# Performance work log

Hardware: AMD Instinct MI355X
Metric: run time of the kernel (lower is better)

Reference implementation:

```python
import jax, jax.numpy as jnp
import numpy as np

N, L, S, E, D = 8, 2048, 2048, 1024, 64

def setup_inputs() -> dict:
    key = jax.random.key(0)
    ks = jax.random.split(key, 6)
    q = jax.random.normal(ks[0], (N, L, E), dtype=jnp.float32)
    k = jax.random.normal(ks[1], (N, S, E), dtype=jnp.float32)
    v = jax.random.normal(ks[2], (N, S, E), dtype=jnp.float32)
    # Linear weights stored as [E, D] so projection is x @ W
    Wq = jax.random.normal(ks[3], (E, D), dtype=jnp.float32) / np.sqrt(E)
    Wk = jax.random.normal(ks[4], (E, D), dtype=jnp.float32) / np.sqrt(E)
    Wv = jax.random.normal(ks[5], (E, D), dtype=jnp.float32) / np.sqrt(E)
    # causal bool mask: True above diagonal => masked to -inf
    attn_mask = jnp.triu(jnp.ones((L, S), dtype=bool), k=1)
    return {"q": q, "k": k, "v": v, "Wq": Wq, "Wk": Wk, "Wv": Wv, "attn_mask": attn_mask}


def reference(q, k, v, Wq, Wk, Wv, attn_mask):
    qh = q @ Wq                      # [N, L, D]
    kh = k @ Wk                      # [N, S, D]
    vh = v @ Wv                      # [N, S, D]
    # NOTE: source divides by d**(-1/2), i.e. multiplies by sqrt(D) (faithful bug)
    scale = jnp.asarray(D, dtype=qh.dtype) ** 0.5
    scores = jnp.einsum("nld,nsd->nls", qh, kh) * scale   # [N, L, S]
    scores = jnp.where(attn_mask[None, :, :], -jnp.inf, scores)
    weights = jax.nn.softmax(scores, axis=-1)
    out = jnp.einsum("nls,nsd->nld", weights, vh)          # [N, L, D]
    return out
```

## Files before the change

kernel.cpp:

```cpp
#include <hip/hip_runtime.h>
#include <math.h>

#define NB 8
#define LQ 2048
#define LOG2E 1.44269504088896f

typedef __attribute__((ext_vector_type(4))) float f32x4;
typedef __attribute__((ext_vector_type(8))) short s16x8;

__device__ __forceinline__ unsigned f2bf_u(float f) {
  unsigned u = __builtin_bit_cast(unsigned, f);
  u += 0x7FFFu + ((u >> 16) & 1u);
  return u >> 16;
}
__device__ __forceinline__ float bf2f(unsigned h) {
  unsigned u = h << 16;
  return __builtin_bit_cast(float, u);
}

#define MFMA16 __builtin_amdgcn_mfma_f32_16x16x32_bf16

__global__ __launch_bounds__(256) void wsplit_kernel(
    const float* __restrict__ Wq, const float* __restrict__ Wk,
    const float* __restrict__ Wv, short* __restrict__ wt) {
  int bk = blockIdx.x;
  int z = blockIdx.y;
  const float* W = (z == 0) ? Wq : (z == 1) ? Wk : Wv;
  __shared__ float tile[64][65];
  int t = threadIdx.x;
#pragma unroll
  for (int it = 0; it < 16; ++it) {
    int kk = it * 4 + (t >> 6);
    int d = t & 63;
    tile[kk][d] = W[(size_t)(bk * 64 + kk) * 64 + d];
  }
  __syncthreads();
#pragma unroll
  for (int it = 0; it < 16; ++it) {
    int d = it * 4 + (t >> 6);
    int kk = t & 63;
    float f = tile[kk][d];
    unsigned h = f2bf_u(f);
    unsigned l = f2bf_u(f - bf2f(h));
    wt[((size_t)(z * 2 + 0) * 64 + d) * 1024 + bk * 64 + kk] = (short)h;
    wt[((size_t)(z * 2 + 1) * 64 + d) * 1024 + bk * 64 + kk] = (short)l;
  }
}

__global__ __launch_bounds__(256, 3) void proj_kernel(
    const float* __restrict__ xq, const float* __restrict__ xk,
    const float* __restrict__ xv, const short* __restrict__ wt,
    short* __restrict__ qhi, short* __restrict__ qlo,
    short* __restrict__ khi, short* __restrict__ klo,
    short* __restrict__ vhT) {
  int z = blockIdx.y;
  const float* x = (z == 0) ? xq : (z == 1) ? xk : xv;
  const short* wthi = wt + (size_t)(z * 2 + 0) * 64 * 1024;
  const short* wtlo = wt + (size_t)(z * 2 + 1) * 64 * 1024;
  int row0 = blockIdx.x * 64;
  int t = threadIdx.x;
  int wv = t >> 6, lane = t & 63;
  int c = lane & 15, quad = lane >> 4;

  __shared__ float xa[2][64 * 64];
  __shared__ short vtile[64][72];

  const float* xg = x + (size_t)row0 * 1024;

#define STAGE(buf, kb)                                                        \
  {                                                                           \
    _Pragma("unroll") for (int j = 0; j < 4; ++j) {                           \
      int row = wv * 16 + j * 4 + quad;                                       \
      const float* src = xg + (size_t)row * 1024 + (kb) * 64 +                \
                         ((c ^ (row & 7)) << 2);                              \
      float* dst = &xa[buf][(wv * 4 + j) * 256];       \
      __builtin_amdgcn_global_load_lds(                                       \
          (const __attribute__((address_space(1))) unsigned*)src,             \
          (__attribute__((address_space(3))) unsigned*)dst, 16, 0, 0);        \
    }                                                                         \
  }

  f32x4 acc[4] = {};
  STAGE(0, 0);
  __syncthreads();
  int cur = 0;
  int rowl = wv * 16 + c;
  for (int kb = 0; kb < 16; ++kb) {
    if (kb < 15) STAGE(cur ^ 1, kb + 1);
    s16x8 bh[4][2], bl[4][2];
    int ko = kb * 64 + quad * 8;
#pragma unroll
    for (int cs = 0; cs < 4; ++cs) {
      const short* bp = wthi + (size_t)(cs * 16 + c) * 1024 + ko;
      const short* lp = wtlo + (size_t)(cs * 16 + c) * 1024 + ko;
      bh[cs][0] = *(const s16x8*)(bp);
      bh[cs][1] = *(const s16x8*)(bp + 32);
      bl[cs][0] = *(const s16x8*)(lp);
      bl[cs][1] = *(const s16x8*)(lp + 32);
    }
    const float* arow = &xa[cur][rowl * 64];
#pragma unroll
    for (int kc = 0; kc < 2; ++kc) {
      int ch0 = ((kc * 8 + quad * 2 + 0) ^ (c & 7)) << 2;
      int ch1 = ((kc * 8 + quad * 2 + 1) ^ (c & 7)) << 2;
      f32x4 a0 = *(const f32x4*)(arow + ch0);
      f32x4 a1 = *(const f32x4*)(arow + ch1);
      s16x8 ah, al;
#pragma unroll
      for (int j = 0; j < 4; ++j) {
        unsigned h;
        h = f2bf_u(a0[j]); ah[j] = (short)h;     al[j] = (short)f2bf_u(a0[j] - bf2f(h));
        h = f2bf_u(a1[j]); ah[4 + j] = (short)h; al[4 + j] = (short)f2bf_u(a1[j] - bf2f(h));
      }
#pragma unroll
      for (int cs = 0; cs < 4; ++cs) {
        acc[cs] = MFMA16(ah, bh[cs][kc], acc[cs], 0, 0, 0);
        acc[cs] = MFMA16(ah, bl[cs][kc], acc[cs], 0, 0, 0);
        acc[cs] = MFMA16(al, bh[cs][kc], acc[cs], 0, 0, 0);
      }
    }
    __syncthreads();
    cur ^= 1;
  }
#undef STAGE
  if (z < 2) {
    short* hi = (z == 0) ? qhi : khi;
    short* lo = (z == 0) ? qlo : klo;
#pragma unroll
    for (int cs = 0; cs < 4; ++cs)
#pragma unroll
      for (int r = 0; r < 4; ++r) {
        int row = row0 + wv * 16 + quad * 4 + r;
        int col = cs * 16 + c;
        float val = acc[cs][r];
        unsigned h = f2bf_u(val);
        unsigned l = f2bf_u(val - bf2f(h));
        hi[(size_t)row * 64 + col] = (short)h;
        lo[(size_t)row * 64 + col] = (short)l;
      }
  } else {
#pragma unroll
    for (int cs = 0; cs < 4; ++cs)
#pragma unroll
      for (int r = 0; r < 4; ++r)
        vtile[cs * 16 + c][wv * 16 + quad * 4 + r] = (short)f2bf_u(acc[cs][r]);
    __syncthreads();
    int n = row0 >> 11;
    int sbase = row0 & 2047;
    int d = t >> 2, sc = (t & 3) * 16;
#pragma unroll
    for (int j = 0; j < 2; ++j) {
      s16x8 vv = *(const s16x8*)&vtile[d][sc + j * 8];
      *(s16x8*)&vhT[((size_t)n * 64 + d) * LQ + sbase + sc + j * 8] = vv;
    }
  }
}

__global__ __launch_bounds__(256, 3) void attn_kernel(
    const short* __restrict__ qhi, const short* __restrict__ qlo,
    const short* __restrict__ khi, const short* __restrict__ klo,
    const short* __restrict__ vhT, float* __restrict__ outp) {
  int bid = blockIdx.x;
  int n = bid & 7;
  int qt = 127 - (bid >> 3);
  int t = threadIdx.x;
  int wv = t >> 6, lane = t & 63;
  int c = lane & 15, quad = lane >> 4;
  int qr0 = qt * 16;
  __shared__ short pS[4][16][72];
  __shared__ float mS[4][16], lS[4][16];
  __shared__ float oS[4][16][64];
  s16x8 qfh[2], qfl[2];
  size_t qbase = ((size_t)n * LQ + qr0 + c) * 64;
#pragma unroll
  for (int kc = 0; kc < 2; ++kc) {
    qfh[kc] = *(const s16x8*)&qhi[qbase + kc * 32 + quad * 8];
    qfl[kc] = *(const s16x8*)&qlo[qbase + kc * 32 + quad * 8];
  }
  f32x4 o[4] = {};
  float m_r[4], l_r[4];
#pragma unroll
  for (int r = 0; r < 4; ++r) { m_r[r] = -INFINITY; l_r[r] = 0.0f; }
  int ktmax = qt >> 2;
  for (int kt = wv; kt <= ktmax; kt += 4) {
    int s0 = kt * 64;
    size_t kbase = ((size_t)n * LQ + s0) * 64;
    f32x4 sa[4] = {};
#pragma unroll
    for (int ct = 0; ct < 4; ++ct) {
      size_t rb = kbase + (size_t)(ct * 16 + c) * 64;
#pragma unroll
      for (int kc = 0; kc < 2; ++kc) {
        s16x8 bh = *(const s16x8*)&khi[rb + kc * 32 + quad * 8];
        s16x8 bl = *(const s16x8*)&klo[rb + kc * 32 + quad * 8];
        sa[ct] = MFMA16(qfh[kc], bh, sa[ct], 0, 0, 0);
        sa[ct] = MFMA16(qfh[kc], bl, sa[ct], 0, 0, 0);
        sa[ct] = MFMA16(qfl[kc], bh, sa[ct], 0, 0, 0);
      }
    }
    s16x8 vb[4][2];
#pragma unroll
    for (int dt = 0; dt < 4; ++dt)
#pragma unroll
      for (int kc2 = 0; kc2 < 2; ++kc2)
        vb[dt][kc2] = *(const s16x8*)&vhT[((size_t)n * 64 + dt * 16 + c) * LQ +
                                          s0 + kc2 * 32 + quad * 8];
    float sv[4][4];
    bool diag = (kt == ktmax);
#pragma unroll
    for (int ct = 0; ct < 4; ++ct)
#pragma unroll
      for (int r = 0; r < 4; ++r) {
        float xsc = sa[ct][r] * 8.0f;
        if (diag) {
          int sg = s0 + ct * 16 + c;
          int qg = qr0 + quad * 4 + r;
          if (sg > qg) xsc = -INFINITY;
        }
        sv[ct][r] = xsc;
      }
    float alpha[4];
#pragma unroll
    for (int r = 0; r < 4; ++r) {
      float mx = fmaxf(fmaxf(sv[0][r], sv[1][r]), fmaxf(sv[2][r], sv[3][r]));
#pragma unroll
      for (int off = 1; off < 16; off <<= 1) mx = fmaxf(mx, __shfl_xor(mx, off, 64));
      float mnew = fmaxf(m_r[r], mx);
      alpha[r] = exp2f((m_r[r] - mnew) * LOG2E);
      m_r[r] = mnew;
      float rs = 0.0f;
#pragma unroll
      for (int ct = 0; ct < 4; ++ct) {
        float p = exp2f((sv[ct][r] - mnew) * LOG2E);
        sv[ct][r] = p;
        rs += p;
      }
#pragma unroll
      for (int off = 1; off < 16; off <<= 1) rs += __shfl_xor(rs, off, 64);
      l_r[r] = l_r[r] * alpha[r] + rs;
    }
#pragma unroll
    for (int dt = 0; dt < 4; ++dt)
#pragma unroll
      for (int r = 0; r < 4; ++r) o[dt][r] *= alpha[r];
#pragma unroll
    for (int ct = 0; ct < 4; ++ct)
#pragma unroll
      for (int r = 0; r < 4; ++r)
        pS[wv][quad * 4 + r][ct * 16 + c] = (short)f2bf_u(sv[ct][r]);
    s16x8 pa[2];
#pragma unroll
    for (int kc2 = 0; kc2 < 2; ++kc2)
      pa[kc2] = *(const s16x8*)&pS[wv][c][kc2 * 32 + quad * 8];
#pragma unroll
    for (int dt = 0; dt < 4; ++dt)
#pragma unroll
      for (int kc2 = 0; kc2 < 2; ++kc2)
        o[dt] = MFMA16(pa[kc2], vb[dt][kc2], o[dt], 0, 0, 0);
  }
#pragma unroll
  for (int dt = 0; dt < 4; ++dt)
#pragma unroll
    for (int r = 0; r < 4; ++r)
      oS[wv][quad * 4 + r][dt * 16 + c] = o[dt][r];
  if (c == 0) {
#pragma unroll
    for (int r = 0; r < 4; ++r) {
      mS[wv][quad * 4 + r] = m_r[r];
      lS[wv][quad * 4 + r] = l_r[r];
    }
  }
  __syncthreads();
  {
    int r = t >> 4;
    int c4 = (t & 15) * 4;
    float m0 = mS[0][r], m1 = mS[1][r], m2 = mS[2][r], m3 = mS[3][r];
    float mstar = fmaxf(fmaxf(m0, m1), fmaxf(m2, m3));
    float s0 = exp2f((m0 - mstar) * LOG2E);
    float s1 = exp2f((m1 - mstar) * LOG2E);
    float s2 = exp2f((m2 - mstar) * LOG2E);
    float s3 = exp2f((m3 - mstar) * LOG2E);
    float lstar = s0 * lS[0][r] + s1 * lS[1][r] + s2 * lS[2][r] + s3 * lS[3][r];
    float inv = 1.0f / lstar;
    f32x4 oa;
#pragma unroll
    for (int j = 0; j < 4; ++j)
      oa[j] = (s0 * oS[0][r][c4 + j] + s1 * oS[1][r][c4 + j] +
               s2 * oS[2][r][c4 + j] + s3 * oS[3][r][c4 + j]) * inv;
    *(f32x4*)&outp[((size_t)n * LQ + qr0 + r) * 64 + c4] = oa;
  }
}

extern "C" void kernel_launch(void* const* d_in, const int* in_sizes, int n_in,
                              void* d_out, int out_size, void* d_ws, size_t ws_size,
                              hipStream_t stream) {
  const float* q = (const float*)d_in[0];
  const float* k = (const float*)d_in[1];
  const float* v = (const float*)d_in[2];
  const float* Wq = (const float*)d_in[3];
  const float* Wk = (const float*)d_in[4];
  const float* Wv = (const float*)d_in[5];
  float* out = (float*)d_out;

  char* ws = (char*)d_ws;
  short* wt  = (short*)ws;
  short* qhi = (short*)(ws + 786432);
  short* qlo = qhi + (size_t)16384 * 64;
  short* khi = qlo + (size_t)16384 * 64;
  short* klo = khi + (size_t)16384 * 64;
  short* vhT = klo + (size_t)16384 * 64;

  wsplit_kernel<<<dim3(16, 3), 256, 0, stream>>>(Wq, Wk, Wv, wt);
  proj_kernel<<<dim3(256, 3), 256, 0, stream>>>(q, k, v, wt, qhi, qlo, khi, klo, vhT);
  attn_kernel<<<dim3(1024), 256, 0, stream>>>(qhi, qlo, khi, klo, vhT, out);
}
```

Baseline: 310.3 us.

## Pre-swizzle split weights and stage them through shared memory in projection

```diff
diff --git a/kernel.cpp b/kernel.cpp
--- a/kernel.cpp
+++ b/kernel.cpp
@@ -7,6 +7,7 @@
 
 typedef __attribute__((ext_vector_type(4))) float f32x4;
 typedef __attribute__((ext_vector_type(8))) short s16x8;
+typedef __attribute__((ext_vector_type(4))) int i32x4;
 
 __device__ __forceinline__ unsigned f2bf_u(float f) {
   unsigned u = __builtin_bit_cast(unsigned, f);
@@ -42,8 +43,12 @@
     float f = tile[kk][d];
     unsigned h = f2bf_u(f);
     unsigned l = f2bf_u(f - bf2f(h));
-    wt[((size_t)(z * 2 + 0) * 64 + d) * 1024 + bk * 64 + kk] = (short)h;
-    wt[((size_t)(z * 2 + 1) * 64 + d) * 1024 + bk * 64 + kk] = (short)l;
+    int cs = d >> 4, cc = d & 15;
+    int kc = kk >> 5, qd = (kk >> 3) & 3, j = kk & 7;
+    size_t base = (size_t)z * 131072 + (size_t)bk * 8192 +
+                  (size_t)(cs * 2 + kc) * 512 + (size_t)(qd * 16 + cc) * 8 + j;
+    wt[base] = (short)h;
+    wt[base + 4096] = (short)l;
   }
 }
 
@@ -55,25 +60,25 @@
     short* __restrict__ vhT) {
   int z = blockIdx.y;
   const float* x = (z == 0) ? xq : (z == 1) ? xk : xv;
-  const short* wthi = wt + (size_t)(z * 2 + 0) * 64 * 1024;
-  const short* wtlo = wt + (size_t)(z * 2 + 1) * 64 * 1024;
+  const char* wb = (const char*)(wt + (size_t)z * 131072);
   int row0 = blockIdx.x * 64;
   int t = threadIdx.x;
   int wv = t >> 6, lane = t & 63;
   int c = lane & 15, quad = lane >> 4;
 
-  __shared__ float xa[2][64 * 64];
-  __shared__ short vtile[64][72];
+  __shared__ __align__(16) float xa[2][4096];
+  __shared__ __align__(16) short bs[8192];
+  char* bsb = (char*)bs;
 
   const float* xg = x + (size_t)row0 * 1024;
 
-#define STAGE(buf, kb)                                                        \
+#define STAGE_A(buf, kb)                                                      \
   {                                                                           \
     _Pragma("unroll") for (int j = 0; j < 4; ++j) {                           \
       int row = wv * 16 + j * 4 + quad;                                       \
       const float* src = xg + (size_t)row * 1024 + (kb) * 64 +                \
                          ((c ^ (row & 7)) << 2);                              \
-      float* dst = &xa[buf][(wv * 4 + j) * 256];       \
+      float* dst = &xa[buf][(wv * 4 + j) * 256];                              \
       __builtin_amdgcn_global_load_lds(                                       \
           (const __attribute__((address_space(1))) unsigned*)src,             \
           (__attribute__((address_space(3))) unsigned*)dst, 16, 0, 0);        \
@@ -81,48 +86,68 @@
   }
 
   f32x4 acc[4] = {};
-  STAGE(0, 0);
+  i32x4 breg[4];
+  STAGE_A(0, 0);
+#pragma unroll
+  for (int i = 0; i < 4; ++i)
+    breg[i] = *(const i32x4*)(wb + i * 4096 + t * 16);
+#pragma unroll
+  for (int i = 0; i < 4; ++i)
+    *(i32x4*)(bsb + i * 4096 + t * 16) = breg[i];
   __syncthreads();
+
   int cur = 0;
   int rowl = wv * 16 + c;
   for (int kb = 0; kb < 16; ++kb) {
-    if (kb < 15) STAGE(cur ^ 1, kb + 1);
+    if (kb < 15) {
+      STAGE_A(cur ^ 1, kb + 1);
+#pragma unroll
+      for (int i = 0; i < 4; ++i)
+        breg[i] = *(const i32x4*)(wb + (size_t)(kb + 1) * 16384 + i * 4096 + t * 16);
+    }
     s16x8 bh[4][2], bl[4][2];
-    int ko = kb * 64 + quad * 8;
-#pragma unroll
-    for (int cs = 0; cs < 4; ++cs) {
-      const short* bp = wthi + (size_t)(cs * 16 + c) * 1024 + ko;
-      const short* lp = wtlo + (size_t)(cs * 16 + c) * 1024 + ko;
-      bh[cs][0] = *(const s16x8*)(bp);
-      bh[cs][1] = *(const s16x8*)(bp + 32);
-      bl[cs][0] = *(const s16x8*)(lp);
-      bl[cs][1] = *(const s16x8*)(lp + 32);
-    }
+#pragma unroll
+    for (int cs = 0; cs < 4; ++cs)
+#pragma unroll
+      for (int kc = 0; kc < 2; ++kc) {
+        bh[cs][kc] = *(const s16x8*)(bsb + (cs * 2 + kc) * 1024 + lane * 16);
+        bl[cs][kc] = *(const s16x8*)(bsb + 8192 + (cs * 2 + kc) * 1024 + lane * 16);
+      }
     const float* arow = &xa[cur][rowl * 64];
+    s16x8 ah[2], al[2];
 #pragma unroll
     for (int kc = 0; kc < 2; ++kc) {
       int ch0 = ((kc * 8 + quad * 2 + 0) ^ (c & 7)) << 2;
       int ch1 = ((kc * 8 + quad * 2 + 1) ^ (c & 7)) << 2;
       f32x4 a0 = *(const f32x4*)(arow + ch0);
       f32x4 a1 = *(const f32x4*)(arow + ch1);
-      s16x8 ah, al;
 #pragma unroll
       for (int j = 0; j < 4; ++j) {
         unsigned h;
-        h = f2bf_u(a0[j]); ah[j] = (short)h;     al[j] = (short)f2bf_u(a0[j] - bf2f(h));
-        h = f2bf_u(a1[j]); ah[4 + j] = (short)h; al[4 + j] = (short)f2bf_u(a1[j] - bf2f(h));
-      }
+        h = f2bf_u(a0[j]); ah[kc][j] = (short)h;
+        al[kc][j] = (short)f2bf_u(a0[j] - bf2f(h));
+        h = f2bf_u(a1[j]); ah[kc][4 + j] = (short)h;
+        al[kc][4 + j] = (short)f2bf_u(a1[j] - bf2f(h));
+      }
+    }
+    __syncthreads();
+    if (kb < 15) {
+#pragma unroll
+      for (int i = 0; i < 4; ++i)
+        *(i32x4*)(bsb + i * 4096 + t * 16) = breg[i];
+    }
+#pragma unroll
+    for (int kc = 0; kc < 2; ++kc)
 #pragma unroll
       for (int cs = 0; cs < 4; ++cs) {
-        acc[cs] = MFMA16(ah, bh[cs][kc], acc[cs], 0, 0, 0);
-        acc[cs] = MFMA16(ah, bl[cs][kc], acc[cs], 0, 0, 0);
-        acc[cs] = MFMA16(al, bh[cs][kc], acc[cs], 0, 0, 0);
-      }
-    }
+        acc[cs] = MFMA16(ah[kc], bh[cs][kc], acc[cs], 0, 0, 0);
+        acc[cs] = MFMA16(ah[kc], bl[cs][kc], acc[cs], 0, 0, 0);
+        acc[cs] = MFMA16(al[kc], bh[cs][kc], acc[cs], 0, 0, 0);
+      }
     __syncthreads();
     cur ^= 1;
   }
-#undef STAGE
+#undef STAGE_A
   if (z < 2) {
     short* hi = (z == 0) ? qhi : khi;
     short* lo = (z == 0) ? qlo : klo;
@@ -139,6 +164,7 @@
         lo[(size_t)row * 64 + col] = (short)l;
       }
   } else {
+    short(*vtile)[72] = (short(*)[72])bs;
 #pragma unroll
     for (int cs = 0; cs < 4; ++cs)
 #pragma unroll
```

Result: faster. 270.7 us (-12.7%).
